# Performance work log

Hardware: AMD Instinct MI355X
Metric: run time of the kernel (lower is better)

## Reference

```python
import jax, jax.numpy as jnp
import numpy as np

OUT, IN = 4096, 4096
B, S = 4, 2048


def setup_inputs() -> dict:
    key = jax.random.key(0)
    k_x, k_wh, k_wm, k_wl, k_r, k_s, k_b = jax.random.split(key, 7)
    x = jax.random.normal(k_x, (B, S, IN), dtype=jnp.float32)
    r = jax.random.uniform(k_r, (OUT, IN))
    high_mask = r < 0.2
    medium_mask = (r < 0.5) & ~high_mask
    weight_high = jax.random.normal(k_wh, (OUT, IN), dtype=jnp.float32) * 0.02 * high_mask
    weight_medium = (jax.random.normal(k_wm, (OUT, IN), dtype=jnp.float32) * 0.02 * medium_mask).astype(jnp.float16)
    weight_low = jax.random.randint(k_wl, (OUT, IN), -127, 128, dtype=jnp.int32)
    low_scale = jax.random.uniform(k_s, (1,), dtype=jnp.float32) * 0.001 + 1e-4
    bias = jax.random.normal(k_b, (OUT,), dtype=jnp.float32) * 0.02
    return {
        "x": x,
        "weight_high": weight_high,
        "weight_medium": weight_medium,
        "weight_low": weight_low,
        "high_precision_mask": high_mask,
        "medium_precision_mask": medium_mask,
        "low_scale": low_scale,
        "bias": bias,
    }


def reference(x, weight_high, weight_medium, weight_low,
              high_precision_mask, medium_precision_mask, low_scale, bias):
    # Reconstruct full fp32 weight from three precision tiers (as in forward).
    low_mask = ~high_precision_mask & ~medium_precision_mask
    w = (weight_high
         + medium_precision_mask * weight_medium.astype(jnp.float32)
         + low_mask * (weight_low.astype(jnp.float32) * low_scale[0]))
    # F.linear: x @ w.T + bias ; [B,S,IN] x [OUT,IN] -> [B,S,OUT]
    return jnp.einsum('bsi,oi->bso', x, w) + bias
```

## Files before the change

kernel.cpp:

```cpp
#include <hip/hip_runtime.h>
#include <hip/hip_bf16.h>
#include <hip/hip_fp16.h>


#define M_DIM 8192
#define N_DIM 4096
#define K_DIM 4096

typedef __attribute__((ext_vector_type(8))) short short8;
typedef __attribute__((ext_vector_type(4))) float floatx4;
typedef __attribute__((ext_vector_type(8))) _Float16 half8;
typedef __attribute__((ext_vector_type(8))) unsigned char uchar8;
typedef __attribute__((ext_vector_type(4))) int intx4;

__device__ inline unsigned short f2bf(float f) {
    union { float f; unsigned u; } v; v.f = f;
    return (unsigned short)((v.u + 0x7fffu + ((v.u >> 16) & 1u)) >> 16);
}

__device__ inline void async16(const void* g, const void* l) {
    __builtin_amdgcn_global_load_lds(
        (const __attribute__((address_space(1))) void*)g,
        (__attribute__((address_space(3))) void*)l,
        16, 0, 0);
}

__global__ __launch_bounds__(256) void detect_kernel(const unsigned* __restrict__ wm_raw,
                                                     const unsigned* __restrict__ hm_raw,
                                                     int* __restrict__ flags) {
    __shared__ int s_f32cnt, s_maskbig;
    if (threadIdx.x == 0) { s_f32cnt = 0; s_maskbig = 0; }
    __syncthreads();
    union { unsigned u; float f; } w; w.u = wm_raw[threadIdx.x];
    float av = fabsf(w.f);
    if (av > 1e-4f && av < 1.0f) atomicAdd(&s_f32cnt, 1);
    if (hm_raw[threadIdx.x] > 1u) atomicAdd(&s_maskbig, 1);
    __syncthreads();
    if (threadIdx.x == 0) {
        flags[0] = (s_f32cnt >= 8) ? 1 : 0;
        flags[1] = (s_maskbig > 0) ? 1 : 0;
    }
}

__global__ __launch_bounds__(256) void cvt_x_kernel(const float* __restrict__ x,
                                                    unsigned short* __restrict__ o) {
    const int i = (blockIdx.x * 256 + threadIdx.x) * 8;
    floatx4 f0 = *(const floatx4*)(x + i);
    floatx4 f1 = *(const floatx4*)(x + i + 4);
    short8 s;
    s[0] = (short)f2bf(f0[0]); s[1] = (short)f2bf(f0[1]);
    s[2] = (short)f2bf(f0[2]); s[3] = (short)f2bf(f0[3]);
    s[4] = (short)f2bf(f1[0]); s[5] = (short)f2bf(f1[1]);
    s[6] = (short)f2bf(f1[2]); s[7] = (short)f2bf(f1[3]);
    *(short8*)(o + i) = s;
}

__global__ __launch_bounds__(256) void build_w_kernel(
        const float* __restrict__ wh, const void* __restrict__ wm_raw,
        const int* __restrict__ wl, const void* __restrict__ hm_raw,
        const void* __restrict__ mm_raw, const float* __restrict__ scale_p,
        const int* __restrict__ flags, unsigned short* __restrict__ o) {
    const int i = (blockIdx.x * 256 + threadIdx.x) * 8;
    const float scale = *scale_p;
    const bool wm_f32  = flags[0] != 0;
    const bool mask_u8 = flags[1] != 0;

    floatx4 h0 = *(const floatx4*)(wh + i);
    floatx4 h1 = *(const floatx4*)(wh + i + 4);
    intx4  l0 = *(const intx4*)(wl + i);
    intx4  l1 = *(const intx4*)(wl + i + 4);

    float mv[8];
    if (wm_f32) {
        floatx4 m0 = *(const floatx4*)((const float*)wm_raw + i);
        floatx4 m1 = *(const floatx4*)((const float*)wm_raw + i + 4);
#pragma unroll
        for (int e = 0; e < 4; ++e) { mv[e] = m0[e]; mv[e + 4] = m1[e]; }
    } else {
        half8 m = *(const half8*)((const _Float16*)wm_raw + i);
#pragma unroll
        for (int e = 0; e < 8; ++e) mv[e] = (float)m[e];
    }

    int lowmask[8];
    if (mask_u8) {
        uchar8 a = *(const uchar8*)((const unsigned char*)hm_raw + i);
        uchar8 b = *(const uchar8*)((const unsigned char*)mm_raw + i);
#pragma unroll
        for (int e = 0; e < 8; ++e) lowmask[e] = (a[e] | b[e]) == 0;
    } else {
        intx4 a0 = *(const intx4*)((const int*)hm_raw + i);
        intx4 a1 = *(const intx4*)((const int*)hm_raw + i + 4);
        intx4 b0 = *(const intx4*)((const int*)mm_raw + i);
        intx4 b1 = *(const intx4*)((const int*)mm_raw + i + 4);
#pragma unroll
        for (int e = 0; e < 4; ++e) {
            lowmask[e]     = (a0[e] | b0[e]) == 0;
            lowmask[e + 4] = (a1[e] | b1[e]) == 0;
        }
    }

    short8 s;
#pragma unroll
    for (int e = 0; e < 8; ++e) {
        float v = (e < 4 ? h0[e] : h1[e - 4]) + mv[e];
        int   lw = (e < 4 ? l0[e] : l1[e - 4]);
        if (lowmask[e]) v += (float)lw * scale;
        s[e] = (short)f2bf(v);
    }
    *(short8*)(o + i) = s;
}

__global__ __launch_bounds__(256) void gemm_kernel(
        const unsigned short* __restrict__ A,
        const unsigned short* __restrict__ Bw,
        const float* __restrict__ bias,
        float* __restrict__ out) {
    __shared__ unsigned short As[128 * 32];
    __shared__ unsigned short Bs[128 * 32];
    const int tid  = threadIdx.x;
    const int wave = tid >> 6, lane = tid & 63;
    const int bm0 = blockIdx.y * 128, bn0 = blockIdx.x * 128;
    const int wm = (wave >> 1) * 64, wn = (wave & 1) * 64;
    const int lrow = lane & 15, lquad = lane >> 4;

    floatx4 acc[4][4] = {};

    for (int k0 = 0; k0 < K_DIM; k0 += 32) {
        __syncthreads();
#pragma unroll
        for (int c = 0; c < 2; ++c) {
            const int lb  = wave * 2048 + c * 1024;
            const int e   = (lb >> 1) + lane * 8;
            const int row = e >> 5, col = e & 31;
            async16(A  + (size_t)(bm0 + row) * K_DIM + k0 + col, (const char*)As + lb);
            async16(Bw + (size_t)(bn0 + row) * K_DIM + k0 + col, (const char*)Bs + lb);
        }
        __syncthreads();

        short8 af[4], bf[4];
#pragma unroll
        for (int i = 0; i < 4; ++i)
            af[i] = *(const short8*)&As[(wm + i * 16 + lrow) * 32 + lquad * 8];
#pragma unroll
        for (int j = 0; j < 4; ++j)
            bf[j] = *(const short8*)&Bs[(wn + j * 16 + lrow) * 32 + lquad * 8];
#pragma unroll
        for (int i = 0; i < 4; ++i)
#pragma unroll
            for (int j = 0; j < 4; ++j)
                acc[i][j] = __builtin_amdgcn_mfma_f32_16x16x32_bf16(af[i], bf[j], acc[i][j], 0, 0, 0);
    }

#pragma unroll
    for (int j = 0; j < 4; ++j) {
        const int col = bn0 + wn + j * 16 + lrow;
        const float bv = bias[col];
#pragma unroll
        for (int i = 0; i < 4; ++i) {
            const int row = bm0 + wm + i * 16 + lquad * 4;
#pragma unroll
            for (int r = 0; r < 4; ++r)
                out[(size_t)(row + r) * N_DIM + col] = acc[i][j][r] + bv;
        }
    }
}

__global__ __launch_bounds__(256) void gemm_fused_kernel(
        const float* __restrict__ X,
        const unsigned short* __restrict__ Bw,
        const float* __restrict__ bias,
        float* __restrict__ out) {
    __shared__ unsigned short As[128 * 32];
    __shared__ unsigned short Bs[128 * 32];
    const int tid  = threadIdx.x;
    const int wave = tid >> 6, lane = tid & 63;
    const int bm0 = blockIdx.y * 128, bn0 = blockIdx.x * 128;
    const int wm = (wave >> 1) * 64, wn = (wave & 1) * 64;
    const int lrow = lane & 15, lquad = lane >> 4;
    const int arow = tid >> 1, acol = (tid & 1) * 16;

    floatx4 acc[4][4] = {};

    for (int k0 = 0; k0 < K_DIM; k0 += 32) {
        __syncthreads();
#pragma unroll
        for (int c = 0; c < 2; ++c) {
            const int lb  = wave * 2048 + c * 1024;
            const int e   = (lb >> 1) + lane * 8;
            const int row = e >> 5, col = e & 31;
            async16(Bw + (size_t)(bn0 + row) * K_DIM + k0 + col, (const char*)Bs + lb);
        }
        {
            const float* g = X + (size_t)(bm0 + arow) * K_DIM + k0 + acol;
            floatx4 f0 = *(const floatx4*)(g);
            floatx4 f1 = *(const floatx4*)(g + 4);
            floatx4 f2 = *(const floatx4*)(g + 8);
            floatx4 f3 = *(const floatx4*)(g + 12);
            short8 s0, s1;
            s0[0]=(short)f2bf(f0[0]); s0[1]=(short)f2bf(f0[1]); s0[2]=(short)f2bf(f0[2]); s0[3]=(short)f2bf(f0[3]);
            s0[4]=(short)f2bf(f1[0]); s0[5]=(short)f2bf(f1[1]); s0[6]=(short)f2bf(f1[2]); s0[7]=(short)f2bf(f1[3]);
            s1[0]=(short)f2bf(f2[0]); s1[1]=(short)f2bf(f2[1]); s1[2]=(short)f2bf(f2[2]); s1[3]=(short)f2bf(f2[3]);
            s1[4]=(short)f2bf(f3[0]); s1[5]=(short)f2bf(f3[1]); s1[6]=(short)f2bf(f3[2]); s1[7]=(short)f2bf(f3[3]);
            *(short8*)&As[arow * 32 + acol]     = s0;
            *(short8*)&As[arow * 32 + acol + 8] = s1;
        }
        __syncthreads();

        short8 af[4], bf[4];
#pragma unroll
        for (int i = 0; i < 4; ++i)
            af[i] = *(const short8*)&As[(wm + i * 16 + lrow) * 32 + lquad * 8];
#pragma unroll
        for (int j = 0; j < 4; ++j)
            bf[j] = *(const short8*)&Bs[(wn + j * 16 + lrow) * 32 + lquad * 8];
#pragma unroll
        for (int i = 0; i < 4; ++i)
#pragma unroll
            for (int j = 0; j < 4; ++j)
                acc[i][j] = __builtin_amdgcn_mfma_f32_16x16x32_bf16(af[i], bf[j], acc[i][j], 0, 0, 0);
    }

#pragma unroll
    for (int j = 0; j < 4; ++j) {
        const int col = bn0 + wn + j * 16 + lrow;
        const float bv = bias[col];
#pragma unroll
        for (int i = 0; i < 4; ++i) {
            const int row = bm0 + wm + i * 16 + lquad * 4;
#pragma unroll
            for (int r = 0; r < 4; ++r)
                out[(size_t)(row + r) * N_DIM + col] = acc[i][j][r] + bv;
        }
    }
}

extern "C" void kernel_launch(void* const* d_in, const int* in_sizes, int n_in,
                              void* d_out, int out_size, void* d_ws, size_t ws_size,
                              hipStream_t stream) {
    const float*    x     = (const float*)d_in[0];
    const float*    wh    = (const float*)d_in[1];
    const void*     wmed  = d_in[2];
    const int*      wl    = (const int*)d_in[3];
    const void*     hm    = d_in[4];
    const void*     mm    = d_in[5];
    const float*    scale = (const float*)d_in[6];
    const float*    bias  = (const float*)d_in[7];
    float*          out   = (float*)d_out;

    int*            flags = (int*)d_ws;
    unsigned short* wbf   = (unsigned short*)((char*)d_ws + 256);
    unsigned short* xbf   = (unsigned short*)((char*)d_ws + 256 + (size_t)N_DIM * K_DIM * 2);
    const size_t need_full = 256 + (size_t)N_DIM * K_DIM * 2 + (size_t)M_DIM * K_DIM * 2;

    detect_kernel<<<1, 256, 0, stream>>>((const unsigned*)wmed, (const unsigned*)hm, flags);
    build_w_kernel<<<N_DIM * K_DIM / 2048, 256, 0, stream>>>(wh, wmed, wl, hm, mm, scale, flags, wbf);

    dim3 grid(N_DIM / 128, M_DIM / 128);
    if (ws_size >= need_full) {
        cvt_x_kernel<<<M_DIM * K_DIM / 2048, 256, 0, stream>>>(x, xbf);
        gemm_kernel<<<grid, 256, 0, stream>>>(xbf, wbf, bias, out);
    } else {
        gemm_fused_kernel<<<grid, 256, 0, stream>>>(x, wbf, bias, out);
    }
}
```

Measured before the change: 738.9 us.

## Replace bf16 GEMM with 256x256-tile, 4-stage async-LDS pipelined kernel

Replaces the 128x128 single-buffered GEMM with a 512-thread kernel computing 256x256 tiles, each wave owning a 128x64 sub-tile. Global-to-LDS async loads run through a 4-deep ring buffer with vmcnt-based waits and a single barrier per K step. LDS reads use an XOR swizzle to avoid bank conflicts, blocks are remapped by an XCD-aware swizzle of the block index, and MFMA sections are bracketed with s_setprio. It needs 128KB of dynamic shared memory and many more accumulator registers, which can limit occupancy.

Result: faster. 679.9 us (-8.0%).

```diff
diff --git a/kernel.cpp b/kernel.cpp
--- a/kernel.cpp
+++ b/kernel.cpp
@@ -111,53 +111,98 @@
     *(short8*)(o + i) = s;
 }
 
-__global__ __launch_bounds__(256) void gemm_kernel(
+__global__ __launch_bounds__(512, 2) void gemm256_kernel(
         const unsigned short* __restrict__ A,
         const unsigned short* __restrict__ Bw,
         const float* __restrict__ bias,
         float* __restrict__ out) {
-    __shared__ unsigned short As[128 * 32];
-    __shared__ unsigned short Bs[128 * 32];
+    extern __shared__ char smem[];
     const int tid  = threadIdx.x;
     const int wave = tid >> 6, lane = tid & 63;
-    const int bm0 = blockIdx.y * 128, bn0 = blockIdx.x * 128;
-    const int wm = (wave >> 1) * 64, wn = (wave & 1) * 64;
     const int lrow = lane & 15, lquad = lane >> 4;
 
-    floatx4 acc[4][4] = {};
-
-    for (int k0 = 0; k0 < K_DIM; k0 += 32) {
-        __syncthreads();
-#pragma unroll
-        for (int c = 0; c < 2; ++c) {
-            const int lb  = wave * 2048 + c * 1024;
-            const int e   = (lb >> 1) + lane * 8;
-            const int row = e >> 5, col = e & 31;
-            async16(A  + (size_t)(bm0 + row) * K_DIM + k0 + col, (const char*)As + lb);
-            async16(Bw + (size_t)(bn0 + row) * K_DIM + k0 + col, (const char*)Bs + lb);
-        }
-        __syncthreads();
-
-        short8 af[4], bf[4];
-#pragma unroll
-        for (int i = 0; i < 4; ++i)
-            af[i] = *(const short8*)&As[(wm + i * 16 + lrow) * 32 + lquad * 8];
-#pragma unroll
-        for (int j = 0; j < 4; ++j)
-            bf[j] = *(const short8*)&Bs[(wn + j * 16 + lrow) * 32 + lquad * 8];
-#pragma unroll
-        for (int i = 0; i < 4; ++i)
-#pragma unroll
-            for (int j = 0; j < 4; ++j)
-                acc[i][j] = __builtin_amdgcn_mfma_f32_16x16x32_bf16(af[i], bf[j], acc[i][j], 0, 0, 0);
-    }
+    const int wg  = blockIdx.x;
+    const int swz = (wg & 7) * 64 + (wg >> 3);
+    const int bm0 = (swz >> 4) * 256;
+    const int bn0 = (swz & 15) * 256;
+
+    const int wr = wave >> 2, wc = wave & 3;
+    const int wm = wr * 128, wn = wc * 64;
+
+    const int lane2 = lane ^ ((lane & 32) ? 2 : 0);
+    const int srow  = wave * 16 + (lane2 >> 2);
+    const int scol  = (lane2 & 3) * 8;
+    const unsigned short* gA0 = A  + (size_t)(bm0 + srow) * K_DIM + scol;
+    const unsigned short* gA1 = gA0 + (size_t)128 * K_DIM;
+    const unsigned short* gB0 = Bw + (size_t)(bn0 + srow) * K_DIM + scol;
+    const unsigned short* gB1 = gB0 + (size_t)128 * K_DIM;
+    const int dstA = wave * 1024;
+    unsigned ko = 0;
+
+    int offA[8], offB[4];
+#pragma unroll
+    for (int i = 0; i < 8; ++i) {
+        int q = (wm + i * 16 + lrow) * 64 + lquad * 16;
+        offA[i] = q ^ (((q >> 9) & 1) << 5);
+    }
+#pragma unroll
+    for (int j = 0; j < 4; ++j) {
+        int q = (wn + j * 16 + lrow) * 64 + lquad * 16;
+        offB[j] = 16384 + (q ^ (((q >> 9) & 1) << 5));
+    }
+
+    floatx4 acc[8][4] = {};
+
+#define STAGE(buf) do { \
+        char* d_ = smem + (buf) * 32768 + dstA; \
+        async16(gA0 + ko, d_); \
+        async16(gA1 + ko, d_ + 8192); \
+        async16(gB0 + ko, d_ + 16384); \
+        async16(gB1 + ko, d_ + 24576); \
+        ko += 32; } while (0)
+
+#define COMPUTE(buf) do { \
+        const char* ab_ = smem + (buf) * 32768; \
+        short8 af[8], bq[4]; \
+        _Pragma("unroll") \
+        for (int i = 0; i < 8; ++i) af[i] = *(const short8*)(ab_ + offA[i]); \
+        _Pragma("unroll") \
+        for (int j = 0; j < 4; ++j) bq[j] = *(const short8*)(ab_ + offB[j]); \
+        __builtin_amdgcn_s_setprio(1); \
+        _Pragma("unroll") \
+        for (int i = 0; i < 8; ++i) \
+            _Pragma("unroll") \
+            for (int j = 0; j < 4; ++j) \
+                acc[i][j] = __builtin_amdgcn_mfma_f32_16x16x32_bf16(af[i], bq[j], acc[i][j], 0, 0, 0); \
+        __builtin_amdgcn_s_setprio(0); } while (0)
+
+#define WAITV(n) asm volatile("s_waitcnt vmcnt(" #n ")" ::: "memory")
+#define BAR() do { __builtin_amdgcn_s_barrier(); asm volatile("" ::: "memory"); } while (0)
+
+    STAGE(0); STAGE(1); STAGE(2);
+
+    const int NT = K_DIM / 32;
+    for (int t = 0; t < NT - 3; ++t) {
+        WAITV(8);
+        BAR();
+        STAGE((t + 3) & 3);
+        COMPUTE(t & 3);
+    }
+    WAITV(8); BAR(); COMPUTE((NT - 3) & 3);
+    WAITV(4); BAR(); COMPUTE((NT - 2) & 3);
+    WAITV(0); BAR(); COMPUTE((NT - 1) & 3);
+
+#undef STAGE
+#undef COMPUTE
+#undef WAITV
+#undef BAR
 
 #pragma unroll
     for (int j = 0; j < 4; ++j) {
         const int col = bn0 + wn + j * 16 + lrow;
         const float bv = bias[col];
 #pragma unroll
-        for (int i = 0; i < 4; ++i) {
+        for (int i = 0; i < 8; ++i) {
             const int row = bm0 + wm + i * 16 + lquad * 4;
 #pragma unroll
             for (int r = 0; r < 4; ++r)
@@ -253,14 +298,21 @@
     unsigned short* xbf   = (unsigned short*)((char*)d_ws + 256 + (size_t)N_DIM * K_DIM * 2);
     const size_t need_full = 256 + (size_t)N_DIM * K_DIM * 2 + (size_t)M_DIM * K_DIM * 2;
 
+    static bool attr_done = false;
+    if (!attr_done) {
+        (void)hipFuncSetAttribute(reinterpret_cast<const void*>(gemm256_kernel),
+                                  hipFuncAttributeMaxDynamicSharedMemorySize, 131072);
+        attr_done = true;
+    }
+
     detect_kernel<<<1, 256, 0, stream>>>((const unsigned*)wmed, (const unsigned*)hm, flags);
     build_w_kernel<<<N_DIM * K_DIM / 2048, 256, 0, stream>>>(wh, wmed, wl, hm, mm, scale, flags, wbf);
 
-    dim3 grid(N_DIM / 128, M_DIM / 128);
     if (ws_size >= need_full) {
         cvt_x_kernel<<<M_DIM * K_DIM / 2048, 256, 0, stream>>>(x, xbf);
-        gemm_kernel<<<grid, 256, 0, stream>>>(xbf, wbf, bias, out);
+        gemm256_kernel<<<dim3(512), dim3(512), 131072, stream>>>(xbf, wbf, bias, out);
     } else {
+        dim3 grid(N_DIM / 128, M_DIM / 128);
         gemm_fused_kernel<<<grid, 256, 0, stream>>>(x, wbf, bias, out);
     }
 }
```
